# Kernel optimization log

Hardware: AMD Instinct MI355X
Metric: run time of the kernel (lower is better)

The kernel has to match this reference:

```python
import jax, jax.numpy as jnp
import numpy as np

INPUT_DIM = 1024
EMBED_DIMS = 128


def setup_inputs() -> dict:
    key = jax.random.key(0)
    ks = jax.random.split(key, 7)
    s_in = 1.0 / np.sqrt(INPUT_DIM)
    x = jax.random.normal(ks[0], (4, 4096, INPUT_DIM), dtype=jnp.float32)
    Wq = jax.random.uniform(ks[1], (INPUT_DIM, EMBED_DIMS), jnp.float32, -s_in, s_in)
    bq = jax.random.uniform(ks[2], (EMBED_DIMS,), jnp.float32, -s_in, s_in)
    Wk = jax.random.uniform(ks[3], (INPUT_DIM, EMBED_DIMS), jnp.float32, -s_in, s_in)
    bk = jax.random.uniform(ks[4], (EMBED_DIMS,), jnp.float32, -s_in, s_in)
    Wv = jax.random.uniform(ks[5], (INPUT_DIM, EMBED_DIMS), jnp.float32, -s_in, s_in)
    bv = jax.random.uniform(ks[6], (EMBED_DIMS,), jnp.float32, -s_in, s_in)
    return {"x": x, "Wq": Wq, "bq": bq, "Wk": Wk, "bk": bk, "Wv": Wv, "bv": bv}


def reference(x, Wq, bq, Wk, bk, Wv, bv):
    # x: [B, L, C]
    Q = jnp.einsum('blc,cd->bld', x, Wq) + bq  # [B, L, D]
    K = jnp.einsum('blc,cd->bld', x, Wk) + bk
    V = jnp.einsum('blc,cd->bld', x, Wv) + bv
    d_k = Q.shape[-1]
    scores = jnp.einsum('bld,bmd->blm', Q, K) / jnp.sqrt(jnp.float32(d_k))  # [B, L, L]
    attn = jax.nn.softmax(scores, axis=-1)
    return jnp.einsum('blm,bmd->bld', attn, V)  # [B, L, D]
```

## Files before the change

kernel.cpp:

```cpp
#include <hip/hip_runtime.h>
#include <stdint.h>

typedef __bf16 bf16;
typedef __bf16 bf16x8 __attribute__((ext_vector_type(8)));
typedef __bf16 bf16x4 __attribute__((ext_vector_type(4)));
typedef _Float16 f16;
typedef f16 f16x8 __attribute__((ext_vector_type(8)));
typedef f16 f16x4 __attribute__((ext_vector_type(4)));
typedef float f32x4 __attribute__((ext_vector_type(4)));

#define LQ    16384
#define CDIM  1024
#define DDIM  128
#define NSPLIT 4
#define QS 0.12751741f

__global__ void prep_kernel(const float* __restrict__ Wq, const float* __restrict__ Wk,
                            const float* __restrict__ Wv, const float* __restrict__ bq,
                            const float* __restrict__ bk, const float* __restrict__ bv,
                            bf16* __restrict__ Wt, float* __restrict__ bias_all) {
  int idx = blockIdx.x * 256 + threadIdx.x;
  int p = idx >> 17;
  int rem = idx & 131071;
  int k = rem >> 7, n = rem & 127;
  const float* W = (p == 0) ? Wq : (p == 1) ? Wk : Wv;
  float s = (p == 0) ? QS : 1.0f;
  Wt[(size_t)(p * 128 + n) * CDIM + k] = (bf16)(W[rem] * s);
  if (idx < 384) {
    int pp = idx >> 7, nn = idx & 127;
    const float* b = (pp == 0) ? bq : (pp == 1) ? bk : bv;
    bias_all[idx] = b[nn] * ((pp == 0) ? QS : 1.0f);
  }
}

__global__ __launch_bounds__(256, 2) void qkv_gemm(
    const float* __restrict__ x, const bf16* __restrict__ Wt,
    const float* __restrict__ bias_all,
    bf16* __restrict__ Qw, bf16* __restrict__ Kw, f16* __restrict__ Vtw) {
  __shared__ bf16 Al[2][128 * 72];
  __shared__ bf16 Bl[2][128 * 72];
  const int t = threadIdx.x;
  const int w = t >> 6;
  const int lane = t & 63;
  const int l15 = lane & 15;
  const int quad = lane >> 4;
  const int lin = blockIdx.y * 128 + blockIdx.x;
  const int logical = (lin & 7) * 48 + (lin >> 3);
  const int y = logical % 3;
  const int m0 = (logical / 3) * 128;
  const bf16* W = Wt + (size_t)y * (DDIM * CDIM);
  const int m_off = (w & 1) * 64;
  const int n_off = (w >> 1) * 64;

  f32x4 zero4 = {0.f, 0.f, 0.f, 0.f};
  f32x4 acc[4][4];
#pragma unroll
  for (int i = 0; i < 4; i++)
#pragma unroll
    for (int j = 0; j < 4; j++) acc[i][j] = zero4;

  const int xrr = t >> 4;
  const int xc = (t & 15) << 2;
  const int wr = t >> 3;
  const int wc = (t & 7) << 3;

  float4 xa[8];
  bf16x8 wa[4];
#pragma unroll
  for (int c = 0; c < 8; c++)
    xa[c] = *(const float4*)&x[(size_t)(m0 + c * 16 + xrr) * CDIM + xc];
#pragma unroll
  for (int c = 0; c < 4; c++)
    wa[c] = *(const bf16x8*)&W[(size_t)(c * 32 + wr) * CDIM + wc];

  for (int kc = 0; kc < 16; kc++) {
    bf16* Ab = Al[kc & 1];
    bf16* Bb = Bl[kc & 1];
#pragma unroll
    for (int c = 0; c < 8; c++) {
      bf16x4 v;
      v[0] = (bf16)xa[c].x; v[1] = (bf16)xa[c].y;
      v[2] = (bf16)xa[c].z; v[3] = (bf16)xa[c].w;
      *(bf16x4*)&Ab[(c * 16 + xrr) * 72 + xc] = v;
    }
#pragma unroll
    for (int c = 0; c < 4; c++)
      *(bf16x8*)&Bb[(c * 32 + wr) * 72 + wc] = wa[c];

    const int kn = (kc < 15 ? kc + 1 : 15) * 64;
#pragma unroll
    for (int c = 0; c < 8; c++)
      xa[c] = *(const float4*)&x[(size_t)(m0 + c * 16 + xrr) * CDIM + kn + xc];
#pragma unroll
    for (int c = 0; c < 4; c++)
      wa[c] = *(const bf16x8*)&W[(size_t)(c * 32 + wr) * CDIM + kn + wc];

    __syncthreads();

#pragma unroll
    for (int ks = 0; ks < 2; ks++) {
      bf16x8 af[4], bfr[4];
#pragma unroll
      for (int mt = 0; mt < 4; mt++)
        af[mt] = *(const bf16x8*)&Ab[(m_off + mt * 16 + l15) * 72 + ks * 32 + quad * 8];
#pragma unroll
      for (int nt = 0; nt < 4; nt++)
        bfr[nt] = *(const bf16x8*)&Bb[(n_off + nt * 16 + l15) * 72 + ks * 32 + quad * 8];
#pragma unroll
      for (int mt = 0; mt < 4; mt++)
#pragma unroll
        for (int nt = 0; nt < 4; nt++)
          acc[mt][nt] = __builtin_amdgcn_mfma_f32_16x16x32_bf16(af[mt], bfr[nt], acc[mt][nt], 0, 0, 0);
    }
  }

  float bias4[4];
#pragma unroll
  for (int nt = 0; nt < 4; nt++) bias4[nt] = bias_all[y * 128 + n_off + nt * 16 + l15];

  if (y < 2) {
    bf16* outp = (y == 0) ? Qw : Kw;
#pragma unroll
    for (int mt = 0; mt < 4; mt++)
#pragma unroll
      for (int nt = 0; nt < 4; nt++) {
        int n = n_off + nt * 16 + l15;
#pragma unroll
        for (int r = 0; r < 4; r++) {
          int m = m0 + m_off + mt * 16 + quad * 4 + r;
          outp[(size_t)m * DDIM + n] = (bf16)(acc[mt][nt][r] + bias4[nt]);
        }
      }
  } else {
#pragma unroll
    for (int mt = 0; mt < 4; mt++)
#pragma unroll
      for (int nt = 0; nt < 4; nt++) {
        int n = n_off + nt * 16 + l15;
        int m = m0 + m_off + mt * 16 + quad * 4;
        f16x4 pv;
#pragma unroll
        for (int r = 0; r < 4; r++) pv[r] = (f16)(acc[mt][nt][r] + bias4[nt]);
        *(f16x4*)&Vtw[(size_t)n * LQ + m] = pv;
      }
  }
}

__global__ __launch_bounds__(256, 2) void flash_kernel(
    const bf16* __restrict__ Qw, const bf16* __restrict__ Kw, const f16* __restrict__ Vtw,
    bf16* __restrict__ Opb, float* __restrict__ lp) {
  __shared__ bf16 Kl[2][64 * 136];
  __shared__ f16  Vl[2][128 * 72];

  const int t = threadIdx.x;
  const int w = t >> 6;
  const int lane = t & 63;
  const int l15 = lane & 15;
  const int quad = lane >> 4;
  const int lin = blockIdx.y * 128 + blockIdx.x;
  const int logical = ((lin & 7) << 6) + (lin >> 3);
  const int qb = logical & 127;
  const int sp = logical >> 7;
  const int batch = qb >> 5;
  const int q0w = qb * 128 + w * 32;
  const int kv_base = batch * 4096 + sp * 1024;

  bf16x8 qf[2][4];
#pragma unroll
  for (int nq = 0; nq < 2; nq++)
#pragma unroll
    for (int ks = 0; ks < 4; ks++)
      qf[nq][ks] = *(const bf16x8*)&Qw[(size_t)(q0w + nq * 16 + l15) * DDIM + ks * 32 + quad * 8];

  f32x4 zero4 = {0.f, 0.f, 0.f, 0.f};
  f32x4 o[2][8];
#pragma unroll
  for (int nq = 0; nq < 2; nq++)
#pragma unroll
    for (int dt = 0; dt < 8; dt++) o[nq][dt] = zero4;
  f32x4 li4[2];
  li4[0] = zero4; li4[1] = zero4;

  f16x4 onef = {(f16)1.f, (f16)1.f, (f16)1.f, (f16)1.f};

  const int kr = t >> 4;
  const int kcol = (t & 15) << 3;
  const int vr = t >> 3;
  const int vcol = (t & 7) << 3;

  bf16x8 ka[4];
  f16x8 va[4];
#pragma unroll
  for (int c = 0; c < 4; c++)
    ka[c] = *(const bf16x8*)&Kw[(size_t)(kv_base + c * 16 + kr) * DDIM + kcol];
#pragma unroll
  for (int c = 0; c < 4; c++)
    va[c] = *(const f16x8*)&Vtw[(size_t)(c * 32 + vr) * LQ + kv_base + vcol];

  for (int tile = 0; tile < 16; tile++) {
    bf16* Kb = Kl[tile & 1];
    f16*  Vb = Vl[tile & 1];
#pragma unroll
    for (int c = 0; c < 4; c++)
      *(bf16x8*)&Kb[(c * 16 + kr) * 136 + kcol] = ka[c];
#pragma unroll
    for (int c = 0; c < 4; c++)
      *(f16x8*)&Vb[(c * 32 + vr) * 72 + vcol] = va[c];

    const int kvn = kv_base + (tile < 15 ? tile + 1 : 15) * 64;
#pragma unroll
    for (int c = 0; c < 4; c++)
      ka[c] = *(const bf16x8*)&Kw[(size_t)(kvn + c * 16 + kr) * DDIM + kcol];
#pragma unroll
    for (int c = 0; c < 4; c++)
      va[c] = *(const f16x8*)&Vtw[(size_t)(c * 32 + vr) * LQ + kvn + vcol];

    __syncthreads();

    f32x4 sv[4][2];
#pragma unroll
    for (int mk = 0; mk < 4; mk++)
#pragma unroll
      for (int nq = 0; nq < 2; nq++) sv[mk][nq] = zero4;
#pragma unroll
    for (int ks = 0; ks < 4; ks++) {
      bf16x8 kf[4];
#pragma unroll
      for (int mk = 0; mk < 4; mk++)
        kf[mk] = *(const bf16x8*)&Kb[(mk * 16 + l15) * 136 + ks * 32 + quad * 8];
      __builtin_amdgcn_s_setprio(1);
#pragma unroll
      for (int mk = 0; mk < 4; mk++)
#pragma unroll
        for (int nq = 0; nq < 2; nq++)
          sv[mk][nq] = __builtin_amdgcn_mfma_f32_16x16x32_bf16(kf[mk], qf[nq][ks], sv[mk][nq], 0, 0, 0);
      __builtin_amdgcn_s_setprio(0);
    }

#pragma unroll
    for (int mk = 0; mk < 4; mk++)
#pragma unroll
      for (int nq = 0; nq < 2; nq++)
#pragma unroll
        for (int r = 0; r < 4; r++)
          sv[mk][nq][r] = exp2f(sv[mk][nq][r]);

#pragma unroll
    for (int s = 0; s < 4; s++) {
      f16x4 pa[2];
#pragma unroll
      for (int nq = 0; nq < 2; nq++) {
        f16x4 p;
#pragma unroll
        for (int r = 0; r < 4; r++) p[r] = (f16)sv[s][nq][r];
        pa[nq] = p;
      }
      f16x4 vfa[8];
#pragma unroll
      for (int dt = 0; dt < 8; dt++)
        vfa[dt] = *(const f16x4*)&Vb[(dt * 16 + l15) * 72 + s * 16 + quad * 4];
      __builtin_amdgcn_s_setprio(1);
#pragma unroll
      for (int dt = 0; dt < 8; dt++)
#pragma unroll
        for (int nq = 0; nq < 2; nq++)
          o[nq][dt] = __builtin_amdgcn_mfma_f32_16x16x16f16(pa[nq], vfa[dt], o[nq][dt], 0, 0, 0);
#pragma unroll
      for (int nq = 0; nq < 2; nq++)
        li4[nq] = __builtin_amdgcn_mfma_f32_16x16x16f16(pa[nq], onef, li4[nq], 0, 0, 0);
      __builtin_amdgcn_s_setprio(0);
    }
  }

  const size_t po = (size_t)sp * LQ * DDIM;
#pragma unroll
  for (int nq = 0; nq < 2; nq++)
#pragma unroll
    for (int dt = 0; dt < 8; dt++)
#pragma unroll
      for (int r = 0; r < 4; r++)
        Opb[po + (size_t)(q0w + nq * 16 + quad * 4 + r) * DDIM + dt * 16 + l15] = (bf16)o[nq][dt][r];
  if (l15 == 0) {
#pragma unroll
    for (int nq = 0; nq < 2; nq++)
#pragma unroll
      for (int r = 0; r < 4; r++)
        lp[(size_t)sp * LQ + q0w + nq * 16 + quad * 4 + r] = li4[nq][r];
  }
}

__global__ void combine_kernel(const bf16* __restrict__ Opb, const float* __restrict__ lp,
                               float* __restrict__ out) {
  int idx = blockIdx.x * 256 + threadIdx.x;
  int q = idx >> 5;
  int d = (idx & 31) * 4;
  float lsum = 0.f;
  float acc[4] = {0.f, 0.f, 0.f, 0.f};
#pragma unroll
  for (int sp = 0; sp < NSPLIT; sp++) {
    lsum += lp[(size_t)sp * LQ + q];
    bf16x4 ov = *(const bf16x4*)&Opb[(size_t)sp * LQ * DDIM + (size_t)q * DDIM + d];
#pragma unroll
    for (int j = 0; j < 4; j++) acc[j] += (float)ov[j];
  }
  float inv = 1.0f / lsum;
  float4 r;
  r.x = acc[0] * inv; r.y = acc[1] * inv; r.z = acc[2] * inv; r.w = acc[3] * inv;
  *(float4*)&out[(size_t)q * DDIM + d] = r;
}

extern "C" void kernel_launch(void* const* d_in, const int* in_sizes, int n_in,
                              void* d_out, int out_size, void* d_ws, size_t ws_size,
                              hipStream_t stream) {
  const float* x  = (const float*)d_in[0];
  const float* Wq = (const float*)d_in[1];
  const float* bq = (const float*)d_in[2];
  const float* Wk = (const float*)d_in[3];
  const float* bk = (const float*)d_in[4];
  const float* Wv = (const float*)d_in[5];
  const float* bv = (const float*)d_in[6];
  char* ws = (char*)d_ws;
  bf16* Qw   = (bf16*)(ws);
  bf16* Kw   = (bf16*)(ws + ((size_t)4 << 20));
  f16*  Vtw  = (f16*)(ws + ((size_t)8 << 20));
  bf16* Wt   = (bf16*)(ws + ((size_t)12 << 20));
  float* bias_all = (float*)(ws + ((size_t)12 << 20) + 786432);
  bf16* Opb  = (bf16*)(ws + ((size_t)13 << 20));
  float* lpp = (float*)(ws + ((size_t)29 << 20));
  float* out = (float*)d_out;

  prep_kernel<<<1536, 256, 0, stream>>>(Wq, Wk, Wv, bq, bk, bv, Wt, bias_all);
  qkv_gemm<<<dim3(128, 3), 256, 0, stream>>>(x, Wt, bias_all, Qw, Kw, Vtw);
  flash_kernel<<<dim3(128, NSPLIT), 256, 0, stream>>>(Qw, Kw, Vtw, Opb, lpp);
  combine_kernel<<<2048, 256, 0, stream>>>(Opb, lpp, out);
}
```

Baseline: 190.4 us.

## Switch flash attention MFMAs to 32x32x16 tiles with permlane P repacking

The flash kernel moves from 16x16 MFMA tiles to 32x32x16 bf16/f16 MFMAs for both the QK^T and PV products. Each wave now holds a single 32-row Q fragment and 32x32 accumulators. The exp'd scores are packed to f16 with cvt_pkrtz and rearranged across lane halves with v_permlane32_swap, so the accumulator layout can feed directly as the A operand without going through LDS. This cuts the MFMA instruction count and the LDS fragment reloads per tile. It uses raw exp2 and round-toward-zero conversion, changes register pressure, and relies on an inline asm instruction specific to gfx950.

```diff
diff --git a/kernel.cpp b/kernel.cpp
--- a/kernel.cpp
+++ b/kernel.cpp
@@ -7,13 +7,20 @@
 typedef _Float16 f16;
 typedef f16 f16x8 __attribute__((ext_vector_type(8)));
 typedef f16 f16x4 __attribute__((ext_vector_type(4)));
+typedef f16 f16x2 __attribute__((ext_vector_type(2)));
 typedef float f32x4 __attribute__((ext_vector_type(4)));
+typedef float f32x16 __attribute__((ext_vector_type(16)));
+typedef uint32_t u32x4 __attribute__((ext_vector_type(4)));
 
 #define LQ    16384
 #define CDIM  1024
 #define DDIM  128
 #define NSPLIT 4
 #define QS 0.12751741f
+
+static __device__ __forceinline__ uint32_t pkrtz(float a, float b) {
+  return __builtin_bit_cast(uint32_t, __builtin_amdgcn_cvt_pkrtz(a, b));
+}
 
 __global__ void prep_kernel(const float* __restrict__ Wq, const float* __restrict__ Wk,
                             const float* __restrict__ Wv, const float* __restrict__ bq,
@@ -155,8 +162,8 @@
   const int t = threadIdx.x;
   const int w = t >> 6;
   const int lane = t & 63;
-  const int l15 = lane & 15;
-  const int quad = lane >> 4;
+  const int l31 = lane & 31;
+  const int hi = lane >> 5;
   const int lin = blockIdx.y * 128 + blockIdx.x;
   const int logical = ((lin & 7) << 6) + (lin >> 3);
   const int qb = logical & 127;
@@ -165,23 +172,19 @@
   const int q0w = qb * 128 + w * 32;
   const int kv_base = batch * 4096 + sp * 1024;
 
-  bf16x8 qf[2][4];
-#pragma unroll
-  for (int nq = 0; nq < 2; nq++)
-#pragma unroll
-    for (int ks = 0; ks < 4; ks++)
-      qf[nq][ks] = *(const bf16x8*)&Qw[(size_t)(q0w + nq * 16 + l15) * DDIM + ks * 32 + quad * 8];
-
-  f32x4 zero4 = {0.f, 0.f, 0.f, 0.f};
-  f32x4 o[2][8];
-#pragma unroll
-  for (int nq = 0; nq < 2; nq++)
-#pragma unroll
-    for (int dt = 0; dt < 8; dt++) o[nq][dt] = zero4;
-  f32x4 li4[2];
-  li4[0] = zero4; li4[1] = zero4;
-
-  f16x4 onef = {(f16)1.f, (f16)1.f, (f16)1.f, (f16)1.f};
+  bf16x8 qf[8];
+#pragma unroll
+  for (int ks = 0; ks < 8; ks++)
+    qf[ks] = *(const bf16x8*)&Qw[(size_t)(q0w + l31) * DDIM + ks * 16 + hi * 8];
+
+  const f32x16 z16 = {0.f,0.f,0.f,0.f,0.f,0.f,0.f,0.f,0.f,0.f,0.f,0.f,0.f,0.f,0.f,0.f};
+  f32x16 o[4];
+  o[0] = z16; o[1] = z16; o[2] = z16; o[3] = z16;
+  f32x16 liacc = z16;
+
+  f16x8 ones;
+#pragma unroll
+  for (int i = 0; i < 8; i++) ones[i] = (f16)1.f;
 
   const int kr = t >> 4;
   const int kcol = (t & 15) << 3;
@@ -217,75 +220,61 @@
 
     __syncthreads();
 
-    f32x4 sv[4][2];
-#pragma unroll
-    for (int mk = 0; mk < 4; mk++)
-#pragma unroll
-      for (int nq = 0; nq < 2; nq++) sv[mk][nq] = zero4;
-#pragma unroll
-    for (int ks = 0; ks < 4; ks++) {
-      bf16x8 kf[4];
-#pragma unroll
-      for (int mk = 0; mk < 4; mk++)
-        kf[mk] = *(const bf16x8*)&Kb[(mk * 16 + l15) * 136 + ks * 32 + quad * 8];
-      __builtin_amdgcn_s_setprio(1);
-#pragma unroll
-      for (int mk = 0; mk < 4; mk++)
-#pragma unroll
-        for (int nq = 0; nq < 2; nq++)
-          sv[mk][nq] = __builtin_amdgcn_mfma_f32_16x16x32_bf16(kf[mk], qf[nq][ks], sv[mk][nq], 0, 0, 0);
-      __builtin_amdgcn_s_setprio(0);
-    }
-
-#pragma unroll
-    for (int mk = 0; mk < 4; mk++)
-#pragma unroll
-      for (int nq = 0; nq < 2; nq++)
-#pragma unroll
-        for (int r = 0; r < 4; r++)
-          sv[mk][nq][r] = exp2f(sv[mk][nq][r]);
-
-#pragma unroll
-    for (int s = 0; s < 4; s++) {
-      f16x4 pa[2];
-#pragma unroll
-      for (int nq = 0; nq < 2; nq++) {
-        f16x4 p;
-#pragma unroll
-        for (int r = 0; r < 4; r++) p[r] = (f16)sv[s][nq][r];
-        pa[nq] = p;
+    f32x16 sv0 = z16, sv1 = z16;
+    __builtin_amdgcn_s_setprio(1);
+#pragma unroll
+    for (int ks = 0; ks < 8; ks++) {
+      bf16x8 kf0 = *(const bf16x8*)&Kb[l31 * 136 + ks * 16 + hi * 8];
+      bf16x8 kf1 = *(const bf16x8*)&Kb[(32 + l31) * 136 + ks * 16 + hi * 8];
+      sv0 = __builtin_amdgcn_mfma_f32_32x32x16_bf16(kf0, qf[ks], sv0, 0, 0, 0);
+      sv1 = __builtin_amdgcn_mfma_f32_32x32x16_bf16(kf1, qf[ks], sv1, 0, 0, 0);
+    }
+    __builtin_amdgcn_s_setprio(0);
+
+#pragma unroll
+    for (int r = 0; r < 16; r++) {
+      sv0[r] = __builtin_amdgcn_exp2f(sv0[r]);
+      sv1[r] = __builtin_amdgcn_exp2f(sv1[r]);
+    }
+
+#pragma unroll
+    for (int mk = 0; mk < 2; mk++) {
+      const f32x16 s = mk ? sv1 : sv0;
+#pragma unroll
+      for (int h = 0; h < 2; h++) {
+        const int b = h * 8;
+        uint32_t a0 = pkrtz(s[b + 0], s[b + 1]);
+        uint32_t a1 = pkrtz(s[b + 2], s[b + 3]);
+        uint32_t a2 = pkrtz(s[b + 4], s[b + 5]);
+        uint32_t a3 = pkrtz(s[b + 6], s[b + 7]);
+        asm("v_permlane32_swap_b32 %0, %1" : "+v"(a0), "+v"(a2));
+        asm("v_permlane32_swap_b32 %0, %1" : "+v"(a1), "+v"(a3));
+        u32x4 aw; aw.x = a0; aw.y = a1; aw.z = a2; aw.w = a3;
+        f16x8 pa = __builtin_bit_cast(f16x8, aw);
+        __builtin_amdgcn_s_setprio(1);
+#pragma unroll
+        for (int dt = 0; dt < 4; dt++) {
+          f16x8 vf = *(const f16x8*)&Vb[(dt * 32 + l31) * 72 + mk * 32 + h * 16 + hi * 8];
+          o[dt] = __builtin_amdgcn_mfma_f32_32x32x16_f16(pa, vf, o[dt], 0, 0, 0);
+        }
+        liacc = __builtin_amdgcn_mfma_f32_32x32x16_f16(pa, ones, liacc, 0, 0, 0);
+        __builtin_amdgcn_s_setprio(0);
       }
-      f16x4 vfa[8];
-#pragma unroll
-      for (int dt = 0; dt < 8; dt++)
-        vfa[dt] = *(const f16x4*)&Vb[(dt * 16 + l15) * 72 + s * 16 + quad * 4];
-      __builtin_amdgcn_s_setprio(1);
-#pragma unroll
-      for (int dt = 0; dt < 8; dt++)
-#pragma unroll
-        for (int nq = 0; nq < 2; nq++)
-          o[nq][dt] = __builtin_amdgcn_mfma_f32_16x16x16f16(pa[nq], vfa[dt], o[nq][dt], 0, 0, 0);
-#pragma unroll
-      for (int nq = 0; nq < 2; nq++)
-        li4[nq] = __builtin_amdgcn_mfma_f32_16x16x16f16(pa[nq], onef, li4[nq], 0, 0, 0);
-      __builtin_amdgcn_s_setprio(0);
     }
   }
 
   const size_t po = (size_t)sp * LQ * DDIM;
 #pragma unroll
-  for (int nq = 0; nq < 2; nq++)
-#pragma unroll
-    for (int dt = 0; dt < 8; dt++)
-#pragma unroll
-      for (int r = 0; r < 4; r++)
-        Opb[po + (size_t)(q0w + nq * 16 + quad * 4 + r) * DDIM + dt * 16 + l15] = (bf16)o[nq][dt][r];
-  if (l15 == 0) {
-#pragma unroll
-    for (int nq = 0; nq < 2; nq++)
-#pragma unroll
-      for (int r = 0; r < 4; r++)
-        lp[(size_t)sp * LQ + q0w + nq * 16 + quad * 4 + r] = li4[nq][r];
+  for (int dt = 0; dt < 4; dt++)
+#pragma unroll
+    for (int r = 0; r < 16; r++) {
+      int q = q0w + (r & 3) + 8 * (r >> 2) + 4 * hi;
+      Opb[po + (size_t)q * DDIM + dt * 32 + l31] = (bf16)o[dt][r];
+    }
+  if (l31 == 0) {
+#pragma unroll
+    for (int r = 0; r < 16; r++)
+      lp[(size_t)sp * LQ + q0w + (r & 3) + 8 * (r >> 2) + 4 * hi] = liacc[r];
   }
 }
 
```

Result: faster. 180.7 us (-5.1%).
